# Kernel tuning notes

Hardware: AMD Instinct MI355X
Metric: run time of the kernel (lower is better)

Reference implementation:

```python
import jax, jax.numpy as jnp
import numpy as np

D_MODEL = 512
N_HEADS = 8
D_K = D_MODEL // N_HEADS
MAX_LEN = 512  # max_seq_len; rel table has 2*MAX_LEN-1 rows


def setup_inputs() -> dict:
    key = jax.random.key(0)
    ks = jax.random.split(key, 7)
    B, S = 8, 512
    s = 1.0 / np.sqrt(D_MODEL)
    return {
        "x": jax.random.normal(ks[0], (B, S, D_MODEL), jnp.float32),
        "Wq": jax.random.normal(ks[1], (D_MODEL, D_MODEL), jnp.float32) * s,
        "bq": jnp.zeros((D_MODEL,), jnp.float32),
        "Wk": jax.random.normal(ks[2], (D_MODEL, D_MODEL), jnp.float32) * s,
        "bk": jnp.zeros((D_MODEL,), jnp.float32),
        "Wv": jax.random.normal(ks[3], (D_MODEL, D_MODEL), jnp.float32) * s,
        "bv": jnp.zeros((D_MODEL,), jnp.float32),
        "Wo": jax.random.normal(ks[4], (D_MODEL, D_MODEL), jnp.float32) * s,
        "bo": jnp.zeros((D_MODEL,), jnp.float32),
        "rel_embed": jax.random.normal(ks[5], (2 * MAX_LEN - 1, D_MODEL), jnp.float32) * 0.02,
    }


def reference(x, Wq, bq, Wk, bk, Wv, bv, Wo, bo, rel_embed):
    B, S, _ = x.shape
    scale = np.sqrt(D_K).astype(np.float32)

    def split_heads(t):  # (B,S,D) -> (B,H,S,dk)
        return t.reshape(B, S, N_HEADS, D_K).transpose(0, 2, 1, 3)

    q = split_heads(x @ Wq.T + bq)
    k = split_heads(x @ Wk.T + bk)
    v = split_heads(x @ Wv.T + bv)

    scores = jnp.einsum('bhqd,bhkd->bhqk', q, k) / scale

    # relative position bias: idx[q_pos, k_pos] = k_pos - q_pos + MAX_LEN - 1
    pos = jnp.arange(S)
    rel_idx = pos[None, :] - pos[:, None] + (MAX_LEN - 1)  # (S,S)
    rel_bias = rel_embed[rel_idx].reshape(S, S, N_HEADS, D_K)  # (S,S,H,dk)
    scores = scores + jnp.einsum('bhqd,qkhd->bhqk', q, rel_bias)

    attn = jax.nn.softmax(scores, axis=-1)
    out = jnp.einsum('bhqk,bhkd->bhqd', attn, v)  # (B,H,S,dk)
    out = out.transpose(0, 2, 1, 3).reshape(B, S, D_MODEL)
    return out @ Wo.T + bo
```

## Files before the change

### kernel.cpp

```cpp
#include <hip/hip_runtime.h>
#include <math.h>

#define B_  8
#define S_  512
#define D_  512
#define H_  8
#define DK_ 64

typedef __attribute__((ext_vector_type(8))) short short8;
typedef __attribute__((ext_vector_type(4))) float f32x4;

#define MFMA_BF16(a, b, c) __builtin_amdgcn_mfma_f32_16x16x32_bf16(a, b, c, 0, 0, 0)

__device__ __forceinline__ unsigned bf16_rne(float x) {
    unsigned u = __float_as_uint(x);
    return (u + 0x7FFFu + ((u >> 16) & 1u)) >> 16;
}
__device__ __forceinline__ float bf16f(unsigned h) { return __uint_as_float(h << 16); }

__device__ __forceinline__ void glds16(const ushort* g, ushort* l) {
    __builtin_amdgcn_global_load_lds(
        (const __attribute__((address_space(1))) unsigned int*)g,
        (__attribute__((address_space(3))) unsigned int*)l,
        16, 0, 0);
}

__global__ __launch_bounds__(256)
void conv_pl(const float* __restrict__ x,
             const float* __restrict__ wq, const float* __restrict__ wk,
             const float* __restrict__ wv, const float* __restrict__ wo,
             const float* __restrict__ rel,
             ushort* __restrict__ Xh, ushort* __restrict__ Xl,
             ushort* __restrict__ Wqh, ushort* __restrict__ Wql,
             ushort* __restrict__ Wkh, ushort* __restrict__ Wkl,
             ushort* __restrict__ Wvh, ushort* __restrict__ Wvl,
             ushort* __restrict__ Woh, ushort* __restrict__ Wol,
             ushort* __restrict__ Rg) {
    const int bid = blockIdx.x;
    if (bid >= 3072) {
        const int idx = (bid - 3072) * 256 + threadIdx.x;
        const int d2 = idx & 31;
        const int rr = (idx >> 5) % 1152;
        const int h  = idx / (1152 * 32);
        unsigned v0 = 0, v1 = 0;
        if (rr >= 64 && rr < 64 + 1023) {
            const float* s = &rel[(size_t)(rr - 64) * 512 + h * 64 + d2 * 2];
            v0 = bf16_rne(s[0]); v1 = bf16_rne(s[1]);
        }
        *(uint*)&Rg[((size_t)h * 1152 + rr) * 64 + d2 * 2] = v0 | (v1 << 16);
        return;
    }
    const float* src; ushort* dh; ushort* dl; int i4;
    if (bid < 2048) {
        src = x; dh = Xh; dl = Xl; i4 = bid * 256 + threadIdx.x;
    } else {
        const int r = bid - 2048;
        const int wsel = r >> 8;
        src = (wsel == 0) ? wq : (wsel == 1) ? wk : (wsel == 2) ? wv : wo;
        dh  = (wsel == 0) ? Wqh : (wsel == 1) ? Wkh : (wsel == 2) ? Wvh : Woh;
        dl  = (wsel == 0) ? Wql : (wsel == 1) ? Wkl : (wsel == 2) ? Wvl : Wol;
        i4 = (r & 255) * 256 + threadIdx.x;
    }
    const float4 v = ((const float4*)src)[i4];
    unsigned h[4], l[4];
    const float* vp = &v.x;
    #pragma unroll
    for (int j = 0; j < 4; ++j) { h[j] = bf16_rne(vp[j]); l[j] = bf16_rne(vp[j] - bf16f(h[j])); }
    ((uint2*)dh)[i4] = make_uint2(h[0] | (h[1] << 16), h[2] | (h[3] << 16));
    ((uint2*)dl)[i4] = make_uint2(l[0] | (l[1] << 16), l[2] | (l[3] << 16));
}

template<int XB, int OM>
__global__ __launch_bounds__(256, 3)
void gemm_mfma(const ushort* __restrict__ Xhp, const ushort* __restrict__ Xlp,
               const ushort* __restrict__ Yh0, const ushort* __restrict__ Yl0,
               const ushort* __restrict__ Yh1, const ushort* __restrict__ Yl1,
               const float* __restrict__ bias0, const float* __restrict__ bias1,
               float scale0, float scale1,
               float* __restrict__ outF,
               ushort* __restrict__ oh0, ushort* __restrict__ ol0,
               ushort* __restrict__ oh1, ushort* __restrict__ ol1) {
    __shared__ ushort Xs[2][2][64 * 64];
    __shared__ ushort Ys[2][64 * 64];

    const int z = blockIdx.z;
    const ushort* Yhp = z ? Yh1 : Yh0;
    const float*  bias = z ? bias1 : bias0;
    const float   scale = z ? scale1 : scale0;
    ushort* ohp = z ? oh1 : oh0;
    ushort* olp = z ? ol1 : ol0;

    const int tid = threadIdx.x;
    const int w = tid >> 6, lane = tid & 63;
    const int g = lane >> 4, c = lane & 15;
    const int rloc = lane >> 3, cc8 = lane & 7;
    const int cp = cc8 ^ rloc;
    const int r0 = blockIdx.y * 64;
    const int c0 = blockIdx.x * 64;

    const f32x4 fz = {0.f, 0.f, 0.f, 0.f};
    f32x4 acc[2][2] = {{fz, fz}, {fz, fz}};

    auto stage = [&](int kt, int buf) {
        const int k0 = kt * 64;
        #pragma unroll
        for (int j = 0; j < 6; ++j) {
            const int seg = w * 6 + j;
            const int p = seg >> 3;
            const int rgrp = seg & 7;
            const int row = rgrp * 8 + rloc;
            const ushort* gb;
            if (p == 2) {
                gb = Yhp + (size_t)(c0 + row) * 512 + k0 + cp * 8;
            } else {
                const ushort* Xp = p ? Xlp : Xhp;
                if (XB == 0) {
                    gb = Xp + (size_t)(r0 + row) * 512 + k0 + cp * 8;
                } else {
                    const int b = r0 >> 9, s0 = r0 & 511, hh = k0 >> 6;
                    gb = Xp + (((size_t)(b * 8 + hh)) * 512 + s0 + row) * 64 + cp * 8;
                }
            }
            ushort* lb = (p == 2) ? &Ys[buf][0] : &Xs[buf][p][0];
            glds16(gb, lb + rgrp * 512);
        }
    };

    auto compute = [&](int buf) {
        #pragma unroll
        for (int ks = 0; ks < 2; ++ks) {
            short8 axh[2], axl[2], byh[2];
            const int wm = (w >> 1) * 32, wn = (w & 1) * 32;
            #pragma unroll
            for (int t = 0; t < 2; ++t) {
                int row = wm + t * 16 + c;
                int off = row * 64 + (((ks * 4 + g) ^ (row & 7)) * 8);
                axh[t] = *(const short8*)&Xs[buf][0][off];
                axl[t] = *(const short8*)&Xs[buf][1][off];
                row = wn + t * 16 + c;
                off = row * 64 + (((ks * 4 + g) ^ (row & 7)) * 8);
                byh[t] = *(const short8*)&Ys[buf][off];
            }
            #pragma unroll
            for (int tm = 0; tm < 2; ++tm)
                #pragma unroll
                for (int tn = 0; tn < 2; ++tn) {
                    acc[tm][tn] = MFMA_BF16(axh[tm], byh[tn], acc[tm][tn]);
                    acc[tm][tn] = MFMA_BF16(axl[tm], byh[tn], acc[tm][tn]);
                }
        }
    };

    stage(0, 0);
    __syncthreads();
    for (int kt = 0; kt < 8; ++kt) {
        if (kt < 7) stage(kt + 1, (kt + 1) & 1);
        compute(kt & 1);
        __syncthreads();
    }

    const int wm = (w >> 1) * 32, wn = (w & 1) * 32;
    if (OM == 0) {
        #pragma unroll
        for (int tn = 0; tn < 2; ++tn) {
            const int gc = c0 + wn + tn * 16 + c;
            const float bv = bias[gc];
            #pragma unroll
            for (int tm = 0; tm < 2; ++tm)
                #pragma unroll
                for (int i = 0; i < 4; ++i) {
                    const int gr = r0 + wm + tm * 16 + g * 4 + i;
                    outF[(size_t)gr * 512 + gc] = acc[tm][tn][i] + bv;
                }
        }
    } else if (OM == 2) {
        #pragma unroll
        for (int tn = 0; tn < 2; ++tn) {
            const int gc = c0 + wn + tn * 16 + c;
            const int h = gc >> 6, dk = gc & 63;
            const float bv = bias[gc];
            #pragma unroll
            for (int tm = 0; tm < 2; ++tm)
                #pragma unroll
                for (int i = 0; i < 4; ++i) {
                    const int gr = r0 + wm + tm * 16 + g * 4 + i;
                    const int b = gr >> 9, s = gr & 511;
                    const float v = (acc[tm][tn][i] + bv) * scale;
                    const unsigned hb = bf16_rne(v);
                    const size_t a = (((size_t)(b * 8 + h)) * 512 + s) * 64 + dk;
                    ohp[a] = (ushort)hb;
                    if (olp) olp[a] = (ushort)bf16_rne(v - bf16f(hb));
                }
        }
    } else {
        #pragma unroll
        for (int tm = 0; tm < 2; ++tm)
            #pragma unroll
            for (int i = 0; i < 4; ++i) {
                const int gr = r0 + wm + tm * 16 + g * 4 + i;
                const int h = gr >> 6, dk = gr & 63;
                const float bv = bias[gr];
                #pragma unroll
                for (int tn = 0; tn < 2; ++tn) {
                    const int gc = c0 + wn + tn * 16 + c;
                    const int b = gc >> 9, s = gc & 511;
                    const float v = acc[tm][tn][i] + bv;
                    const size_t a = (((size_t)(b * 8 + h)) * 64 + dk) * 512 + s;
                    ohp[a] = (ushort)bf16_rne(v);
                }
            }
    }
}

__global__ __launch_bounds__(256, 4)
void attn_mfma(const ushort* __restrict__ Qhp, const ushort* __restrict__ Qlp,
               const ushort* __restrict__ Khp, const ushort* __restrict__ Vhp,
               const ushort* __restrict__ Rg,
               float* __restrict__ Op0, float* __restrict__ Op1,
               float2* __restrict__ Ml0, float2* __restrict__ Ml1) {
    __shared__ ushort Ksm[64 * 64];
    __shared__ ushort Vsm[64 * 64];
    __shared__ ushort Rsm[128 * 64];

    const int tid  = threadIdx.x;
    const int w    = tid >> 6;
    const int lane = tid & 63;
    const int g    = lane >> 4;
    const int c    = lane & 15;
    const int rloc = lane >> 3, cc8 = lane & 7;
    const int bh   = blockIdx.y;
    const int h    = bh & 7;
    const int z    = blockIdx.z;
    const int qwb  = blockIdx.x * 64;
    const int qw   = qwb + w * 16;

    ushort* Usm = &Rsm[w * 1376];

    float* __restrict__ Op = z ? Op1 : Op0;
    float2* __restrict__ Ml = z ? Ml1 : Ml0;

    const ushort* KhB = Khp + (size_t)bh * 512 * 64;
    const ushort* VhB = Vhp + (size_t)bh * 64 * 512;
    const ushort* RgH = Rg + (size_t)h * 1152 * 64;

    uint4 rv[4];
    auto issue_rel = [&](int kt) {
        const int rbase = kt * 64 - qwb + 512;
        #pragma unroll
        for (int j = 0; j < 4; ++j) {
            const int cd = j * 256 + tid, row = cd >> 3, cc = cd & 7;
            rv[j] = *(const uint4*)&RgH[(size_t)(rbase + row) * 64 + cc * 8];
        }
    };

    issue_rel(z * 4);
    short8 qfh[2], qfl[2];
    #pragma unroll
    for (int ks = 0; ks < 2; ++ks) {
        const size_t qi = ((size_t)bh * 512 + qw + c) * 64 + ks * 32 + g * 8;
        qfh[ks] = *(const short8*)&Qhp[qi];
        qfl[ks] = *(const short8*)&Qlp[qi];
    }

    const f32x4 fz = {0.f, 0.f, 0.f, 0.f};
    f32x4 o[4] = {fz, fz, fz, fz};
    float m = -INFINITY, l = 0.f;

    for (int kt = z * 4; kt < z * 4 + 4; ++kt) {
        const int k0 = kt * 64;
        __syncthreads();

        #pragma unroll
        for (int j = 0; j < 4; ++j) {
            const int cd = j * 256 + tid, row = cd >> 3, cc = cd & 7;
            *(uint4*)&Rsm[row * 64 + ((cc ^ (row & 7)) << 3)] = rv[j];
        }
        if (w < 2) {
            ushort* lb = &Ksm[w * 32 * 64];
            #pragma unroll
            for (int j = 0; j < 4; ++j) {
                const int row = w * 32 + j * 8 + rloc;
                const int tcq = row >> 4, cq = row & 15;
                const int key = ((tcq & 1) << 5) + ((cq >> 2) << 3)
                              + ((tcq >> 1) << 2) + (cq & 3);
                glds16(KhB + (size_t)(k0 + key) * 64 + ((cc8 ^ rloc) << 3),
                       lb + j * 512);
            }
        } else {
            const ushort* gb = VhB + k0 + (size_t)(w - 2) * 32 * 512;
            ushort* lb = &Vsm[(w - 2) * 32 * 64];
            #pragma unroll
            for (int j = 0; j < 4; ++j)
                glds16(gb + (size_t)(j * 8 + rloc) * 512 + ((cc8 ^ rloc) << 3),
                       lb + j * 512);
        }

        if (kt + 1 < z * 4 + 4) {
            issue_rel(kt + 1);
            asm volatile("s_waitcnt vmcnt(4) lgkmcnt(0)" ::: "memory");
        } else {
            asm volatile("s_waitcnt vmcnt(0) lgkmcnt(0)" ::: "memory");
        }
        __builtin_amdgcn_s_barrier();

        f32x4 u[5];
        #pragma unroll
        for (int ut = 0; ut < 5; ++ut) u[ut] = fz;
        #pragma unroll
        for (int ks = 0; ks < 2; ++ks)
            #pragma unroll
            for (int ut = 0; ut < 5; ++ut) {
                const int rl = 48 - 16 * w + c + ut * 16;
                const short8 rf = *(const short8*)
                    &Rsm[rl * 64 + (((ks * 4 + g) ^ (c & 7)) << 3)];
                u[ut] = MFMA_BF16(qfh[ks], rf, u[ut]);
            }

        f32x4 st[4];
        #pragma unroll
        for (int tc = 0; tc < 4; ++tc) st[tc] = fz;
        #pragma unroll
        for (int ks = 0; ks < 2; ++ks)
            #pragma unroll
            for (int tc = 0; tc < 4; ++tc) {
                const int row = tc * 16 + c;
                const int chv = ((ks * 4 + g) ^ (row & 7)) * 8;
                const short8 kh8 = *(const short8*)&Ksm[row * 64 + chv];
                st[tc] = MFMA_BF16(kh8, qfh[ks], st[tc]);
                st[tc] = MFMA_BF16(kh8, qfl[ks], st[tc]);
            }

        __syncthreads();

        #pragma unroll
        for (int ut = 0; ut < 5; ++ut)
            #pragma unroll
            for (int i = 0; i < 4; ++i)
                Usm[(g * 4 + i) * 86 + c + ut * 16] = (ushort)bf16_rne(u[ut][i]);

        asm volatile("s_waitcnt lgkmcnt(0)" ::: "memory");

        #pragma unroll
        for (int tc = 0; tc < 4; ++tc)
            #pragma unroll
            for (int i = 0; i < 4; ++i) {
                const int key = ((tc & 1) << 5) + 8 * g + ((tc >> 1) << 2) + i;
                st[tc][i] += bf16f(Usm[c * 85 + key + 15]);
            }

        float tm = fmaxf(fmaxf(st[0][0], st[0][1]), fmaxf(st[0][2], st[0][3]));
        #pragma unroll
        for (int tc = 1; tc < 4; ++tc) {
            const float t2 = fmaxf(fmaxf(st[tc][0], st[tc][1]),
                                   fmaxf(st[tc][2], st[tc][3]));
            tm = fmaxf(tm, t2);
        }
        tm = fmaxf(tm, __shfl_xor(tm, 16));
        tm = fmaxf(tm, __shfl_xor(tm, 32));
        const float mn = fmaxf(m, tm);
        const float corr = __expf(m - mn);
        m = mn;
        l *= corr;
        #pragma unroll
        for (int dt = 0; dt < 4; ++dt) o[dt] *= corr;

        uint pk[4][2];
        #pragma unroll
        for (int tc = 0; tc < 4; ++tc) {
            const float p0 = __expf(st[tc][0] - mn);
            const float p1 = __expf(st[tc][1] - mn);
            const float p2 = __expf(st[tc][2] - mn);
            const float p3 = __expf(st[tc][3] - mn);
            l += (p0 + p1) + (p2 + p3);
            pk[tc][0] = bf16_rne(p0) | (bf16_rne(p1) << 16);
            pk[tc][1] = bf16_rne(p2) | (bf16_rne(p3) << 16);
        }

        #pragma unroll
        for (int ks = 0; ks < 2; ++ks) {
            union { uint u4[4]; short8 s8; } pb;
            pb.u4[0] = pk[ks][0];
            pb.u4[1] = pk[ks][1];
            pb.u4[2] = pk[ks + 2][0];
            pb.u4[3] = pk[ks + 2][1];
            #pragma unroll
            for (int dt = 0; dt < 4; ++dt) {
                const int row = dt * 16 + c;
                const int chv = ((ks * 4 + g) ^ (row & 7)) * 8;
                const short8 vh8 = *(const short8*)&Vsm[row * 64 + chv];
                o[dt] = MFMA_BF16(vh8, pb.s8, o[dt]);
            }
        }
    }

    float lt = l;
    lt += __shfl_xor(lt, 16);
    lt += __shfl_xor(lt, 32);
    if (lane < 16) Ml[(size_t)bh * 512 + qw + c] = make_float2(m, lt);
    #pragma unroll
    for (int dt = 0; dt < 4; ++dt)
        #pragma unroll
        for (int i = 0; i < 4; ++i)
            Op[((size_t)bh * 64 + dt * 16 + g * 4 + i) * 512 + qw + c] = o[dt][i];
}

__global__ __launch_bounds__(256)
void attn_combine(const float* __restrict__ Op0, const float* __restrict__ Op1,
                  const float2* __restrict__ Ml0, const float2* __restrict__ Ml1,
                  ushort* __restrict__ Oh, ushort* __restrict__ Ol) {
    __shared__ float L0[64][67];
    __shared__ float L1[64][67];
    const int t = threadIdx.x;
    const int bh = blockIdx.y;
    const int s0 = blockIdx.x * 64;
    #pragma unroll
    for (int j = 0; j < 4; ++j) {
        const int d = (t >> 4) + j * 16;
        const int c4 = (t & 15) * 4;
        const size_t ga = ((size_t)bh * 64 + d) * 512 + s0 + c4;
        *(float4*)&L0[d][c4] = *(const float4*)&Op0[ga];
        *(float4*)&L1[d][c4] = *(const float4*)&Op1[ga];
    }
    __syncthreads();
    const int sl = t >> 2;
    const int d0 = (t & 3) * 16;
    const float2 a = Ml0[(size_t)bh * 512 + s0 + sl];
    const float2 b = Ml1[(size_t)bh * 512 + s0 + sl];
    const float mm = fmaxf(a.x, b.x);
    float w0 = __expf(a.x - mm), w1 = __expf(b.x - mm);
    const float inv = 1.0f / (a.y * w0 + b.y * w1);
    w0 *= inv; w1 *= inv;
    const size_t ob = ((size_t)bh * 512 + s0 + sl) * 64 + d0;
    #pragma unroll
    for (int q = 0; q < 4; ++q) {
        unsigned hb[4], lb4[4];
        #pragma unroll
        for (int e = 0; e < 4; ++e) {
            const int dd = q * 4 + e;
            const float v = L0[d0 + dd][sl] * w0 + L1[d0 + dd][sl] * w1;
            hb[e] = bf16_rne(v);
            lb4[e] = bf16_rne(v - bf16f(hb[e]));
        }
        *(uint2*)&Oh[ob + q * 4] = make_uint2(hb[0] | (hb[1] << 16), hb[2] | (hb[3] << 16));
        *(uint2*)&Ol[ob + q * 4] = make_uint2(lb4[0] | (lb4[1] << 16), lb4[2] | (lb4[3] << 16));
    }
}

extern "C" void kernel_launch(void* const* d_in, const int* in_sizes, int n_in,
                              void* d_out, int out_size, void* d_ws, size_t ws_size,
                              hipStream_t stream) {
    const float* x   = (const float*)d_in[0];
    const float* Wq  = (const float*)d_in[1];
    const float* bq  = (const float*)d_in[2];
    const float* Wk  = (const float*)d_in[3];
    const float* bk  = (const float*)d_in[4];
    const float* Wv  = (const float*)d_in[5];
    const float* bv  = (const float*)d_in[6];
    const float* Wo  = (const float*)d_in[7];
    const float* bo  = (const float*)d_in[8];
    const float* rel = (const float*)d_in[9];
    float* out = (float*)d_out;

    const size_t NP = (size_t)B_ * H_ * S_ * DK_;
    const size_t WP = (size_t)D_ * D_;
    ushort* Xh  = (ushort*)d_ws;
    ushort* Xl  = Xh + NP;
    ushort* Wqh = Xl + NP;
    ushort* Wql = Wqh + WP;
    ushort* Wkh = Wql + WP;
    ushort* Wkl = Wkh + WP;
    ushort* Wvh = Wkl + WP;
    ushort* Wvl = Wvh + WP;
    ushort* Woh = Wvl + WP;
    ushort* Wol = Woh + WP;
    ushort* Qh  = Wol + WP;
    ushort* Ql  = Qh + NP;
    ushort* Kh  = Ql + NP;
    ushort* Kl  = Kh + NP;
    ushort* Vh  = Kl + NP;
    ushort* Rg  = Vh + NP;
    float*  Op1 = (float*)(Rg + 589824);
    float2* Ml0 = (float2*)(Op1 + NP);
    float2* Ml1 = Ml0 + 32768;
    float*  Op0 = (float*)d_ws;

    conv_pl<<<4224, 256, 0, stream>>>(x, Wq, Wk, Wv, Wo, rel,
                                      Xh, Xl, Wqh, Wql, Wkh, Wkl, Wvh, Wvl, Woh, Wol, Rg);

    gemm_mfma<0, 2><<<dim3(8, 64, 2), 256, 0, stream>>>(
        Xh, Xl, Wqh, Wql, Wkh, Wkl, bq, bk, 1.0f, 0.125f,
        nullptr, Qh, Ql, Kh, nullptr);
    gemm_mfma<0, 3><<<dim3(64, 8, 1), 256, 0, stream>>>(
        Wvh, Wvl, Xh, Xl, nullptr, nullptr, bv, nullptr, 1.0f, 1.0f,
        nullptr, Vh, nullptr, nullptr, nullptr);

    attn_mfma<<<dim3(8, 64, 2), 256, 0, stream>>>(
        Qh, Ql, Kh, Vh, Rg, Op0, Op1, Ml0, Ml1);

    attn_combine<<<dim3(8, 64), 256, 0, stream>>>(Op0, Op1, Ml0, Ml1, Kh, Kl);

    gemm_mfma<1, 0><<<dim3(8, 64, 1), 256, 0, stream>>>(
        Kh, Kl, Woh, Wol, nullptr, nullptr, bo, nullptr, 1.0f, 1.0f,
        out, nullptr, nullptr, nullptr, nullptr);
}
```

Baseline: 91.69 us.

## Fuse split-K attention halves and combine into one 512-thread block

Both key halves of the split attention now run in a single 512-thread block, one 4-wave group per half with its own shared-memory buffers. The two partial outputs and their max/sum statistics are merged through shared memory inside the block. This removes the separate combine kernel launch and the fp32 partial output round trip through global memory. In exchange the block uses double the LDS, has fewer blocks (512 instead of 1024), and adds an extra block-wide barrier before the merge.

Result: no change. 90.24 us (-1.6%).

```diff
diff --git a/kernel.cpp b/kernel.cpp
--- a/kernel.cpp
+++ b/kernel.cpp
@@ -212,32 +212,30 @@
     }
 }
 
-__global__ __launch_bounds__(256, 4)
-void attn_mfma(const ushort* __restrict__ Qhp, const ushort* __restrict__ Qlp,
-               const ushort* __restrict__ Khp, const ushort* __restrict__ Vhp,
-               const ushort* __restrict__ Rg,
-               float* __restrict__ Op0, float* __restrict__ Op1,
-               float2* __restrict__ Ml0, float2* __restrict__ Ml1) {
-    __shared__ ushort Ksm[64 * 64];
-    __shared__ ushort Vsm[64 * 64];
-    __shared__ ushort Rsm[128 * 64];
+__global__ __launch_bounds__(512, 2)
+void attn_mfma8(const ushort* __restrict__ Qhp, const ushort* __restrict__ Qlp,
+                const ushort* __restrict__ Khp, const ushort* __restrict__ Vhp,
+                const ushort* __restrict__ Rg,
+                ushort* __restrict__ Oh, ushort* __restrict__ Ol) {
+    __shared__ ushort Ksm[2][64 * 64];
+    __shared__ ushort Vsm[2][64 * 64];
+    __shared__ ushort Rsm[2][128 * 64];
 
     const int tid  = threadIdx.x;
     const int w    = tid >> 6;
+    const int half = w >> 2;
+    const int wl   = w & 3;
+    const int tidh = tid & 255;
     const int lane = tid & 63;
     const int g    = lane >> 4;
     const int c    = lane & 15;
     const int rloc = lane >> 3, cc8 = lane & 7;
     const int bh   = blockIdx.y;
     const int h    = bh & 7;
-    const int z    = blockIdx.z;
     const int qwb  = blockIdx.x * 64;
-    const int qw   = qwb + w * 16;
-
-    ushort* Usm = &Rsm[w * 1376];
-
-    float* __restrict__ Op = z ? Op1 : Op0;
-    float2* __restrict__ Ml = z ? Ml1 : Ml0;
+    const int qw   = qwb + wl * 16;
+
+    ushort* Usm = &Rsm[half][wl * 1376];
 
     const ushort* KhB = Khp + (size_t)bh * 512 * 64;
     const ushort* VhB = Vhp + (size_t)bh * 64 * 512;
@@ -248,12 +246,12 @@
         const int rbase = kt * 64 - qwb + 512;
         #pragma unroll
         for (int j = 0; j < 4; ++j) {
-            const int cd = j * 256 + tid, row = cd >> 3, cc = cd & 7;
+            const int cd = j * 256 + tidh, row = cd >> 3, cc = cd & 7;
             rv[j] = *(const uint4*)&RgH[(size_t)(rbase + row) * 64 + cc * 8];
         }
     };
 
-    issue_rel(z * 4);
+    issue_rel(half * 4);
     short8 qfh[2], qfl[2];
     #pragma unroll
     for (int ks = 0; ks < 2; ++ks) {
@@ -266,20 +264,21 @@
     f32x4 o[4] = {fz, fz, fz, fz};
     float m = -INFINITY, l = 0.f;
 
-    for (int kt = z * 4; kt < z * 4 + 4; ++kt) {
+    for (int t = 0; t < 4; ++t) {
+        const int kt = half * 4 + t;
         const int k0 = kt * 64;
         __syncthreads();
 
         #pragma unroll
         for (int j = 0; j < 4; ++j) {
-            const int cd = j * 256 + tid, row = cd >> 3, cc = cd & 7;
-            *(uint4*)&Rsm[row * 64 + ((cc ^ (row & 7)) << 3)] = rv[j];
-        }
-        if (w < 2) {
-            ushort* lb = &Ksm[w * 32 * 64];
+            const int cd = j * 256 + tidh, row = cd >> 3, cc = cd & 7;
+            *(uint4*)&Rsm[half][row * 64 + ((cc ^ (row & 7)) << 3)] = rv[j];
+        }
+        if (wl < 2) {
+            ushort* lb = &Ksm[half][wl * 32 * 64];
             #pragma unroll
             for (int j = 0; j < 4; ++j) {
-                const int row = w * 32 + j * 8 + rloc;
+                const int row = wl * 32 + j * 8 + rloc;
                 const int tcq = row >> 4, cq = row & 15;
                 const int key = ((tcq & 1) << 5) + ((cq >> 2) << 3)
                               + ((tcq >> 1) << 2) + (cq & 3);
@@ -287,15 +286,15 @@
                        lb + j * 512);
             }
         } else {
-            const ushort* gb = VhB + k0 + (size_t)(w - 2) * 32 * 512;
-            ushort* lb = &Vsm[(w - 2) * 32 * 64];
+            const ushort* gb = VhB + k0 + (size_t)(wl - 2) * 32 * 512;
+            ushort* lb = &Vsm[half][(wl - 2) * 32 * 64];
             #pragma unroll
             for (int j = 0; j < 4; ++j)
                 glds16(gb + (size_t)(j * 8 + rloc) * 512 + ((cc8 ^ rloc) << 3),
                        lb + j * 512);
         }
 
-        if (kt + 1 < z * 4 + 4) {
+        if (t + 1 < 4) {
             issue_rel(kt + 1);
             asm volatile("s_waitcnt vmcnt(4) lgkmcnt(0)" ::: "memory");
         } else {
@@ -310,9 +309,9 @@
         for (int ks = 0; ks < 2; ++ks)
             #pragma unroll
             for (int ut = 0; ut < 5; ++ut) {
-                const int rl = 48 - 16 * w + c + ut * 16;
+                const int rl = 48 - 16 * wl + c + ut * 16;
                 const short8 rf = *(const short8*)
-                    &Rsm[rl * 64 + (((ks * 4 + g) ^ (c & 7)) << 3)];
+                    &Rsm[half][rl * 64 + (((ks * 4 + g) ^ (c & 7)) << 3)];
                 u[ut] = MFMA_BF16(qfh[ks], rf, u[ut]);
             }
 
@@ -325,7 +324,7 @@
             for (int tc = 0; tc < 4; ++tc) {
                 const int row = tc * 16 + c;
                 const int chv = ((ks * 4 + g) ^ (row & 7)) * 8;
-                const short8 kh8 = *(const short8*)&Ksm[row * 64 + chv];
+                const short8 kh8 = *(const short8*)&Ksm[half][row * 64 + chv];
                 st[tc] = MFMA_BF16(kh8, qfh[ks], st[tc]);
                 st[tc] = MFMA_BF16(kh8, qfl[ks], st[tc]);
             }
@@ -387,7 +386,7 @@
             for (int dt = 0; dt < 4; ++dt) {
                 const int row = dt * 16 + c;
                 const int chv = ((ks * 4 + g) ^ (row & 7)) * 8;
-                const short8 vh8 = *(const short8*)&Vsm[row * 64 + chv];
+                const short8 vh8 = *(const short8*)&Vsm[half][row * 64 + chv];
                 o[dt] = MFMA_BF16(vh8, pb.s8, o[dt]);
             }
         }
@@ -396,54 +395,42 @@
     float lt = l;
     lt += __shfl_xor(lt, 16);
     lt += __shfl_xor(lt, 32);
-    if (lane < 16) Ml[(size_t)bh * 512 + qw + c] = make_float2(m, lt);
+
+    __syncthreads();
+
+    float* Ob = (float*)&Rsm[half][0];
+    const int qcol = wl * 16 + c;
     #pragma unroll
     for (int dt = 0; dt < 4; ++dt)
         #pragma unroll
         for (int i = 0; i < 4; ++i)
-            Op[((size_t)bh * 64 + dt * 16 + g * 4 + i) * 512 + qw + c] = o[dt][i];
-}
-
-__global__ __launch_bounds__(256)
-void attn_combine(const float* __restrict__ Op0, const float* __restrict__ Op1,
-                  const float2* __restrict__ Ml0, const float2* __restrict__ Ml1,
-                  ushort* __restrict__ Oh, ushort* __restrict__ Ol) {
-    __shared__ float L0[64][67];
-    __shared__ float L1[64][67];
-    const int t = threadIdx.x;
-    const int bh = blockIdx.y;
-    const int s0 = blockIdx.x * 64;
+            Ob[(dt * 16 + g * 4 + i) * 64 + qcol] = o[dt][i];
+    float2* MlB = (float2*)&Ksm[0][0];
+    if (lane < 16) MlB[half * 64 + qcol] = make_float2(m, lt);
+    __syncthreads();
+
+    const int q   = tid >> 3;
+    const int dk0 = (tid & 7) * 8;
+    const float2 a = MlB[q], b2 = MlB[64 + q];
+    const float mm = fmaxf(a.x, b2.x);
+    float w0 = __expf(a.x - mm), w1 = __expf(b2.x - mm);
+    const float inv = 1.0f / (a.y * w0 + b2.y * w1);
+    w0 *= inv; w1 *= inv;
+    const float* O0 = (const float*)&Rsm[0][0];
+    const float* O1 = (const float*)&Rsm[1][0];
+    unsigned hb[8], lb8[8];
     #pragma unroll
-    for (int j = 0; j < 4; ++j) {
-        const int d = (t >> 4) + j * 16;
-        const int c4 = (t & 15) * 4;
-        const size_t ga = ((size_t)bh * 64 + d) * 512 + s0 + c4;
-        *(float4*)&L0[d][c4] = *(const float4*)&Op0[ga];
-        *(float4*)&L1[d][c4] = *(const float4*)&Op1[ga];
-    }
-    __syncthreads();
-    const int sl = t >> 2;
-    const int d0 = (t & 3) * 16;
-    const float2 a = Ml0[(size_t)bh * 512 + s0 + sl];
-    const float2 b = Ml1[(size_t)bh * 512 + s0 + sl];
-    const float mm = fmaxf(a.x, b.x);
-    float w0 = __expf(a.x - mm), w1 = __expf(b.x - mm);
-    const float inv = 1.0f / (a.y * w0 + b.y * w1);
-    w0 *= inv; w1 *= inv;
-    const size_t ob = ((size_t)bh * 512 + s0 + sl) * 64 + d0;
-    #pragma unroll
-    for (int q = 0; q < 4; ++q) {
-        unsigned hb[4], lb4[4];
-        #pragma unroll
-        for (int e = 0; e < 4; ++e) {
-            const int dd = q * 4 + e;
-            const float v = L0[d0 + dd][sl] * w0 + L1[d0 + dd][sl] * w1;
-            hb[e] = bf16_rne(v);
-            lb4[e] = bf16_rne(v - bf16f(hb[e]));
-        }
-        *(uint2*)&Oh[ob + q * 4] = make_uint2(hb[0] | (hb[1] << 16), hb[2] | (hb[3] << 16));
-        *(uint2*)&Ol[ob + q * 4] = make_uint2(lb4[0] | (lb4[1] << 16), lb4[2] | (lb4[3] << 16));
-    }
+    for (int e = 0; e < 8; ++e) {
+        const int d = dk0 + e;
+        const float v = O0[d * 64 + q] * w0 + O1[d * 64 + q] * w1;
+        hb[e] = bf16_rne(v);
+        lb8[e] = bf16_rne(v - bf16f(hb[e]));
+    }
+    const size_t ob = ((size_t)bh * 512 + qwb + q) * 64 + dk0;
+    *(uint4*)&Oh[ob] = make_uint4(hb[0] | (hb[1] << 16), hb[2] | (hb[3] << 16),
+                                  hb[4] | (hb[5] << 16), hb[6] | (hb[7] << 16));
+    *(uint4*)&Ol[ob] = make_uint4(lb8[0] | (lb8[1] << 16), lb8[2] | (lb8[3] << 16),
+                                  lb8[4] | (lb8[5] << 16), lb8[6] | (lb8[7] << 16));
 }
 
 extern "C" void kernel_launch(void* const* d_in, const int* in_sizes, int n_in,
@@ -479,10 +466,8 @@
     ushort* Kl  = Kh + NP;
     ushort* Vh  = Kl + NP;
     ushort* Rg  = Vh + NP;
-    float*  Op1 = (float*)(Rg + 589824);
-    float2* Ml0 = (float2*)(Op1 + NP);
-    float2* Ml1 = Ml0 + 32768;
-    float*  Op0 = (float*)d_ws;
+    ushort* Oh  = Rg + 589824;
+    ushort* Ol  = Oh + NP;
 
     conv_pl<<<4224, 256, 0, stream>>>(x, Wq, Wk, Wv, Wo, rel,
                                       Xh, Xl, Wqh, Wql, Wkh, Wkl, Wvh, Wvl, Woh, Wol, Rg);
@@ -494,12 +479,10 @@
         Wvh, Wvl, Xh, Xl, nullptr, nullptr, bv, nullptr, 1.0f, 1.0f,
         nullptr, Vh, nullptr, nullptr, nullptr);
 
-    attn_mfma<<<dim3(8, 64, 2), 256, 0, stream>>>(
-        Qh, Ql, Kh, Vh, Rg, Op0, Op1, Ml0, Ml1);
-
-    attn_combine<<<dim3(8, 64), 256, 0, stream>>>(Op0, Op1, Ml0, Ml1, Kh, Kl);
+    attn_mfma8<<<dim3(8, 64), 512, 0, stream>>>(
+        Qh, Ql, Kh, Vh, Rg, Oh, Ol);
 
     gemm_mfma<1, 0><<<dim3(8, 64, 1), 256, 0, stream>>>(
-        Kh, Kl, Woh, Wol, nullptr, nullptr, bo, nullptr, 1.0f, 1.0f,
+        Oh, Ol, Woh, Wol, nullptr, nullptr, bo, nullptr, 1.0f, 1.0f,
         out, nullptr, nullptr, nullptr, nullptr);
 }
```
